# Kernel tuning notes

Measured on AMD Instinct MI355X. Metric: run time of the kernel, lower is better.

The kernel has to match this reference:

```python
import jax, jax.numpy as jnp
import numpy as np

B, T, D, H = 4096, 512, 8, 64  # batch, seq_len, input_size, hidden_size


def setup_inputs() -> dict:
    key = jax.random.key(0)
    ks = jax.random.split(key, 11)
    s = lambda k, shape: (jax.random.normal(k, shape, dtype=jnp.float32) * 0.1)
    return {
        "x": jax.random.normal(ks[0], (B, T, D), dtype=jnp.float32),
        # layer 0 (input_size -> H), PyTorch gate order i,f,g,o packed along 4H
        "Wih0": s(ks[1], (4 * H, D)),
        "Whh0": s(ks[2], (4 * H, H)),
        "bih0": s(ks[3], (4 * H,)),
        "bhh0": s(ks[4], (4 * H,)),
        # layer 1 (H -> H)
        "Wih1": s(ks[5], (4 * H, H)),
        "Whh1": s(ks[6], (4 * H, H)),
        "bih1": s(ks[7], (4 * H,)),
        "bhh1": s(ks[8], (4 * H,)),
        # final linear head H -> 1
        "Wfc": s(ks[9], (1, H)),
        "bfc": s(ks[10], (1,)),
    }


def _lstm_layer(x, Wih, Whh, bih, bhh):
    """Single-direction LSTM layer over x:[B,T,Din] -> hs:[B,T,H]."""
    b, t, _ = x.shape
    h_dim = Whh.shape[1]
    # Precompute input contribution for all timesteps (one big GEMM).
    xg = jnp.einsum("btd,gd->btg", x, Wih) + bih + bhh  # [B,T,4H]

    def step(carry, gx_t):
        h, c = carry
        z = gx_t + h @ Whh.T  # [B,4H]
        i, f, g, o = jnp.split(z, 4, axis=-1)
        i = jax.nn.sigmoid(i)
        f = jax.nn.sigmoid(f)
        g = jnp.tanh(g)
        o = jax.nn.sigmoid(o)
        c = f * c + i * g
        h = o * jnp.tanh(c)
        return (h, c), h

    h0 = jnp.zeros((b, h_dim), x.dtype)
    c0 = jnp.zeros((b, h_dim), x.dtype)
    (_, _), hs = jax.lax.scan(step, (h0, c0), jnp.swapaxes(xg, 0, 1))
    return jnp.swapaxes(hs, 0, 1)  # [B,T,H]


def reference(x, Wih0, Whh0, bih0, bhh0, Wih1, Whh1, bih1, bhh1, Wfc, bfc):
    # nn.LSTM with num_layers=2, batch_first=True; dropout inactive in eval.
    h1 = _lstm_layer(x, Wih0, Whh0, bih0, bhh0)
    h2 = _lstm_layer(h1, Wih1, Whh1, bih1, bhh1)
    last = h2[:, -1, :]  # [B,H]
    return last @ Wfc.T + bfc  # [B,1]
```

## Files before the change

### kernel.cpp

```cpp
#include <hip/hip_runtime.h>

#define BTOT 4096
#define TB   512
#define BD   8
#define BSL  16

#define A0TOG  1024
#define A1BASE 2048
#define A1TOG  1024
#define ZBASE  4096
#define XBASE  8192
#define NLDS   24576

typedef __attribute__((ext_vector_type(8))) short  short8;
typedef __attribute__((ext_vector_type(4))) float  f32x4;

static __device__ __forceinline__ unsigned short f2bf(float f) {
    unsigned u = __float_as_uint(f);
    u += 0x7fffu + ((u >> 16) & 1u);
    return (unsigned short)(u >> 16);
}
static __device__ __forceinline__ float bf2f(unsigned short h) {
    return __uint_as_float(((unsigned)h) << 16);
}
static __device__ __forceinline__ unsigned pkbf(float a, float b) {
    unsigned r;
    asm("v_cvt_pk_bf16_f32 %0, %1, %2" : "=v"(r) : "v"(a), "v"(b));
    return r;
}

static __device__ __forceinline__ void gates4(
    const f32x4 ai, const f32x4 af, const f32x4 ag, const f32x4 ao,
    float cc[4], unsigned hp[2])
{
    float h[4];
    #pragma unroll
    for (int r = 0; r < 4; ++r) {
        const float ei = __builtin_amdgcn_exp2f(ai[r]);
        const float ef = __builtin_amdgcn_exp2f(af[r]);
        const float eg = __builtin_amdgcn_exp2f(ag[r]);
        const float eo = __builtin_amdgcn_exp2f(ao[r]);
        const float Ai = 1.f + ei, Af = 1.f + ef, Ag = 1.f + eg, Ao = 1.f + eo;
        const float P    = Ai * Ag;
        const float numer = cc[r] * P + Af * (eg - 1.f);
        const float rD   = __builtin_amdgcn_rcpf(Af * P);
        cc[r] = numer * rD;
        const float ec = __builtin_amdgcn_exp2f(2.88539008f * cc[r]);
        const float rH = __builtin_amdgcn_rcpf(Ao * (ec + 1.f));
        h[r] = (ec - 1.f) * rH;
    }
    hp[0] = pkbf(h[0], h[1]); hp[1] = pkbf(h[2], h[3]);
}

__global__ __launch_bounds__(512, 2) void lstm2_fused(
    const float* __restrict__ x,
    const float* __restrict__ Wih0, const float* __restrict__ Whh0,
    const float* __restrict__ bih0, const float* __restrict__ bhh0,
    const float* __restrict__ Wih1, const float* __restrict__ Whh1,
    const float* __restrict__ bih1, const float* __restrict__ bhh1,
    const float* __restrict__ Wfc,  const float* __restrict__ bfc,
    float* __restrict__ out)
{
    __shared__ __align__(16) unsigned short lds16[NLDS];

    const int tid  = threadIdx.x;
    const int wid  = tid >> 6;
    const int lane = tid & 63;
    const int q    = lane >> 4;
    const int ln   = lane & 15;
    const int rb   = blockIdx.x * BSL;

    const bool L1w = (wid >= 4);
    const int  g   = L1w ? (wid - 4) : wid;
    const int  jc  = g * 16 + ln;

    const float SCI = -1.44269504f;
    const float SCG =  2.88539008f;
    short8 Bf[4][4];
    #pragma unroll
    for (int G = 0; G < 4; ++G) {
        const int n = G * 64 + jc;
        const float sc = (G == 2) ? SCG : SCI;
        #pragma unroll
        for (int ki = 0; ki < 4; ++ki) {
            union { unsigned short u[8]; short8 v; } t;
            #pragma unroll
            for (int j = 0; j < 8; ++j) {
                const int k = ki * 32 + q * 8 + j;
                float wv = 0.0f;
                if (!L1w) {
                    if (ki < 3) {
                        if (k < 64)      wv = Whh0[n * 64 + k];
                        else if (k < 72) wv = Wih0[n * 8 + (k - 64)];
                    }
                } else {
                    if (k < 64)          wv = Wih1[n * 64 + k];
                    else                 wv = Whh1[n * 64 + (k - 64)];
                }
                t.u[j] = f2bf(sc * wv);
            }
            Bf[G][ki] = t.v;
        }
    }
    f32x4 biasv[4];
    #pragma unroll
    for (int G = 0; G < 4; ++G) {
        const int n = G * 64 + jc;
        const float sc = (G == 2) ? SCG : SCI;
        const float b = sc * (L1w ? (bih1[n] + bhh1[n]) : (bih0[n] + bhh0[n]));
        biasv[G] = (f32x4){b, b, b, b};
    }

    {
        unsigned* z = (unsigned*)lds16;
        #pragma unroll
        for (int i = 0; i < 5; ++i) {
            const int id = tid + i * 512;
            if (id < 2112) z[id] = 0;
        }
    }
    const int srow = tid >> 5, su = tid & 31;
    {
        const float* gp = x + (size_t)(rb + srow) * (TB * BD) + su * 16;
        const float4 v0 = ((const float4*)gp)[0];
        const float4 v1 = ((const float4*)gp)[1];
        const float4 v2 = ((const float4*)gp)[2];
        const float4 v3 = ((const float4*)gp)[3];
        uint4 s0, s1;
        s0.x = pkbf(v0.x, v0.y); s0.y = pkbf(v0.z, v0.w);
        s0.z = pkbf(v1.x, v1.y); s0.w = pkbf(v1.z, v1.w);
        s1.x = pkbf(v2.x, v2.y); s1.y = pkbf(v2.z, v2.w);
        s1.z = pkbf(v3.x, v3.y); s1.w = pkbf(v3.z, v3.w);
        const int el = XBASE + (su * 2) * 128 + srow * 8;
        *(uint4*)(lds16 + el)       = s0;
        *(uint4*)(lds16 + el + 128) = s1;
    }
    __syncthreads();

    const int rbase = q * 128 + ln * 8;
    const int wb    = (jc >> 3) * 128 + q * 32 + (jc & 7);
    const int ln8   = ln * 8;
    const int zaddr = ZBASE + ln8;
    int rdA  = rbase;
    int wr0  = A0TOG + wb;
    int rdH0 = rbase;
    int rdH1 = A1BASE + rbase;
    int wrH1 = A1BASE + A1TOG + wb;

    float cc[4] = {0.f, 0.f, 0.f, 0.f};
    float4 px0, px1, px2, px3;

    for (int it = 0; it <= TB; ++it) {
        const int ph = it & 63;
        if (ph == 48 && it + 16 < TB) {
            const int t0 = (it & ~63) + 64;
            const float* gp = x + (size_t)(rb + srow) * (TB * BD) + t0 * BD + su * 16;
            px0 = ((const float4*)gp)[0];
            px1 = ((const float4*)gp)[1];
            px2 = ((const float4*)gp)[2];
            px3 = ((const float4*)gp)[3];
        }
        if (ph == 62 && it + 2 < TB) {
            const int t0 = (it & ~63) + 64;
            uint4 s0, s1;
            s0.x = pkbf(px0.x, px0.y); s0.y = pkbf(px0.z, px0.w);
            s0.z = pkbf(px1.x, px1.y); s0.w = pkbf(px1.z, px1.w);
            s1.x = pkbf(px2.x, px2.y); s1.y = pkbf(px2.z, px2.w);
            s1.z = pkbf(px3.x, px3.y); s1.w = pkbf(px3.z, px3.w);
            const int el = XBASE + ((t0 & 127) + su * 2) * 128 + srow * 8;
            *(uint4*)(lds16 + el)       = s0;
            *(uint4*)(lds16 + el + 128) = s1;
        }

        if (!L1w) {
            if (it < TB) {
                const short8 a0 = *(const short8*)(lds16 + rdA);
                const short8 a1 = *(const short8*)(lds16 + rdA + 512);
                const int xaddr = (q == 0) ? (XBASE + ((it & 127) << 7) + ln8) : zaddr;
                const short8 a2 = *(const short8*)(lds16 + xaddr);

                f32x4 ai = __builtin_amdgcn_mfma_f32_16x16x32_bf16(a0, Bf[0][0], biasv[0], 0, 0, 0);
                f32x4 af = __builtin_amdgcn_mfma_f32_16x16x32_bf16(a0, Bf[1][0], biasv[1], 0, 0, 0);
                f32x4 ag = __builtin_amdgcn_mfma_f32_16x16x32_bf16(a0, Bf[2][0], biasv[2], 0, 0, 0);
                f32x4 ao = __builtin_amdgcn_mfma_f32_16x16x32_bf16(a0, Bf[3][0], biasv[3], 0, 0, 0);
                ai = __builtin_amdgcn_mfma_f32_16x16x32_bf16(a1, Bf[0][1], ai, 0, 0, 0);
                af = __builtin_amdgcn_mfma_f32_16x16x32_bf16(a1, Bf[1][1], af, 0, 0, 0);
                ag = __builtin_amdgcn_mfma_f32_16x16x32_bf16(a1, Bf[2][1], ag, 0, 0, 0);
                ao = __builtin_amdgcn_mfma_f32_16x16x32_bf16(a1, Bf[3][1], ao, 0, 0, 0);
                ai = __builtin_amdgcn_mfma_f32_16x16x32_bf16(a2, Bf[0][2], ai, 0, 0, 0);
                af = __builtin_amdgcn_mfma_f32_16x16x32_bf16(a2, Bf[1][2], af, 0, 0, 0);
                ag = __builtin_amdgcn_mfma_f32_16x16x32_bf16(a2, Bf[2][2], ag, 0, 0, 0);
                ao = __builtin_amdgcn_mfma_f32_16x16x32_bf16(a2, Bf[3][2], ao, 0, 0, 0);

                unsigned hp[2];
                gates4(ai, af, ag, ao, cc, hp);
                lds16[wr0]      = (unsigned short)hp[0];
                lds16[wr0 + 8]  = (unsigned short)(hp[0] >> 16);
                lds16[wr0 + 16] = (unsigned short)hp[1];
                lds16[wr0 + 24] = (unsigned short)(hp[1] >> 16);
            }
        } else {
            if (it >= 1) {
                const short8 a0 = *(const short8*)(lds16 + rdH0);
                const short8 a1 = *(const short8*)(lds16 + rdH0 + 512);
                const short8 a2 = *(const short8*)(lds16 + rdH1);
                const short8 a3 = *(const short8*)(lds16 + rdH1 + 512);

                f32x4 ai = __builtin_amdgcn_mfma_f32_16x16x32_bf16(a0, Bf[0][0], biasv[0], 0, 0, 0);
                f32x4 af = __builtin_amdgcn_mfma_f32_16x16x32_bf16(a0, Bf[1][0], biasv[1], 0, 0, 0);
                f32x4 ag = __builtin_amdgcn_mfma_f32_16x16x32_bf16(a0, Bf[2][0], biasv[2], 0, 0, 0);
                f32x4 ao = __builtin_amdgcn_mfma_f32_16x16x32_bf16(a0, Bf[3][0], biasv[3], 0, 0, 0);
                ai = __builtin_amdgcn_mfma_f32_16x16x32_bf16(a1, Bf[0][1], ai, 0, 0, 0);
                af = __builtin_amdgcn_mfma_f32_16x16x32_bf16(a1, Bf[1][1], af, 0, 0, 0);
                ag = __builtin_amdgcn_mfma_f32_16x16x32_bf16(a1, Bf[2][1], ag, 0, 0, 0);
                ao = __builtin_amdgcn_mfma_f32_16x16x32_bf16(a1, Bf[3][1], ao, 0, 0, 0);
                ai = __builtin_amdgcn_mfma_f32_16x16x32_bf16(a2, Bf[0][2], ai, 0, 0, 0);
                af = __builtin_amdgcn_mfma_f32_16x16x32_bf16(a2, Bf[1][2], af, 0, 0, 0);
                ag = __builtin_amdgcn_mfma_f32_16x16x32_bf16(a2, Bf[2][2], ag, 0, 0, 0);
                ao = __builtin_amdgcn_mfma_f32_16x16x32_bf16(a2, Bf[3][2], ao, 0, 0, 0);
                ai = __builtin_amdgcn_mfma_f32_16x16x32_bf16(a3, Bf[0][3], ai, 0, 0, 0);
                af = __builtin_amdgcn_mfma_f32_16x16x32_bf16(a3, Bf[1][3], af, 0, 0, 0);
                ag = __builtin_amdgcn_mfma_f32_16x16x32_bf16(a3, Bf[2][3], ag, 0, 0, 0);
                ao = __builtin_amdgcn_mfma_f32_16x16x32_bf16(a3, Bf[3][3], ao, 0, 0, 0);

                unsigned hp[2];
                gates4(ai, af, ag, ao, cc, hp);
                lds16[wrH1]      = (unsigned short)hp[0];
                lds16[wrH1 + 8]  = (unsigned short)(hp[0] >> 16);
                lds16[wrH1 + 16] = (unsigned short)hp[1];
                lds16[wrH1 + 24] = (unsigned short)(hp[1] >> 16);
            }
        }
        __syncthreads();
        rdA ^= A0TOG; wr0 ^= A0TOG; rdH0 ^= A0TOG;
        rdH1 ^= A1TOG; wrH1 ^= A1TOG;
    }

    if (tid < BSL) {
        float s = bfc[0];
        #pragma unroll 8
        for (int j = 0; j < 64; ++j)
            s += bf2f(lds16[A1BASE + A1TOG + (j >> 3) * 128 + tid * 8 + (j & 7)]) * Wfc[j];
        out[rb + tid] = s;
    }
}

extern "C" void kernel_launch(void* const* d_in, const int* in_sizes, int n_in,
                              void* d_out, int out_size, void* d_ws, size_t ws_size,
                              hipStream_t stream) {
    const float* x    = (const float*)d_in[0];
    const float* Wih0 = (const float*)d_in[1];
    const float* Whh0 = (const float*)d_in[2];
    const float* bih0 = (const float*)d_in[3];
    const float* bhh0 = (const float*)d_in[4];
    const float* Wih1 = (const float*)d_in[5];
    const float* Whh1 = (const float*)d_in[6];
    const float* bih1 = (const float*)d_in[7];
    const float* bhh1 = (const float*)d_in[8];
    const float* Wfc  = (const float*)d_in[9];
    const float* bfc  = (const float*)d_in[10];
    float* out = (float*)d_out;

    dim3 grid(BTOT / BSL);
    dim3 block(512);
    lstm2_fused<<<grid, block, 0, stream>>>(x, Wih0, Whh0, bih0, bhh0,
                                            Wih1, Whh1, bih1, bhh1, Wfc, bfc, out);
}
```

Measured before the change: 503.6 us.

## Replace per-step block barriers with LDS progress flags and 4-deep h ring buffers

Replaces the per-timestep __syncthreads with per-wave progress counters in LDS that each wave spins on, so layer-0 and layer-1 waves can run decoupled by up to a few steps. Hidden states move to four-slot ring buffers per layer so producers can run ahead without overwriting data still being read. The x prefetch is also remapped so only 256 threads load 4 timesteps each. This trades barrier stalls for spin-polling LDS traffic and extra LDS use, and relies on fences and volatile reads for correctness.

```diff
diff --git a/kernel.cpp b/kernel.cpp
--- a/kernel.cpp
+++ b/kernel.cpp
@@ -5,12 +5,11 @@
 #define BD   8
 #define BSL  16
 
-#define A0TOG  1024
-#define A1BASE 2048
-#define A1TOG  1024
-#define ZBASE  4096
-#define XBASE  8192
-#define NLDS   24576
+#define H1R    4096
+#define ZBASE  8192
+#define PROGEL 8320
+#define XBASE  12288
+#define NLDS   28672
 
 typedef __attribute__((ext_vector_type(8))) short  short8;
 typedef __attribute__((ext_vector_type(4))) float  f32x4;
@@ -27,6 +26,11 @@
     unsigned r;
     asm("v_cvt_pk_bf16_f32 %0, %1, %2" : "=v"(r) : "v"(a), "v"(b));
     return r;
+}
+static __device__ __forceinline__ unsigned min4h(unsigned a, unsigned b) {
+    const unsigned m1 = min(a & 0xffffu, a >> 16);
+    const unsigned m2 = min(b & 0xffffu, b >> 16);
+    return min(m1, m2);
 }
 
 static __device__ __forceinline__ void gates4(
@@ -41,9 +45,9 @@
         const float eg = __builtin_amdgcn_exp2f(ag[r]);
         const float eo = __builtin_amdgcn_exp2f(ao[r]);
         const float Ai = 1.f + ei, Af = 1.f + ef, Ag = 1.f + eg, Ao = 1.f + eo;
-        const float P    = Ai * Ag;
+        const float P = Ai * Ag;
         const float numer = cc[r] * P + Af * (eg - 1.f);
-        const float rD   = __builtin_amdgcn_rcpf(Af * P);
+        const float rD = __builtin_amdgcn_rcpf(Af * P);
         cc[r] = numer * rD;
         const float ec = __builtin_amdgcn_exp2f(2.88539008f * cc[r]);
         const float rH = __builtin_amdgcn_rcpf(Ao * (ec + 1.f));
@@ -113,134 +117,148 @@
 
     {
         unsigned* z = (unsigned*)lds16;
+        z[1536 + tid] = 0;
+        z[3584 + tid] = 0;
+        if (tid < 64) z[4096 + tid] = 0;
+        if (tid < 4)
+            z[4160 + tid] = (tid >= 2) ? 0x00010001u : 0u;
+    }
+    const int srow = (tid >> 4) & 15, su = tid & 15;
+    if (tid < 256) {
+        const float* gp = x + (size_t)(rb + srow) * (TB * BD) + (su * 4) * BD;
+        float4 v[8];
         #pragma unroll
-        for (int i = 0; i < 5; ++i) {
-            const int id = tid + i * 512;
-            if (id < 2112) z[id] = 0;
-        }
-    }
-    const int srow = tid >> 5, su = tid & 31;
-    {
-        const float* gp = x + (size_t)(rb + srow) * (TB * BD) + su * 16;
-        const float4 v0 = ((const float4*)gp)[0];
-        const float4 v1 = ((const float4*)gp)[1];
-        const float4 v2 = ((const float4*)gp)[2];
-        const float4 v3 = ((const float4*)gp)[3];
-        uint4 s0, s1;
-        s0.x = pkbf(v0.x, v0.y); s0.y = pkbf(v0.z, v0.w);
-        s0.z = pkbf(v1.x, v1.y); s0.w = pkbf(v1.z, v1.w);
-        s1.x = pkbf(v2.x, v2.y); s1.y = pkbf(v2.z, v2.w);
-        s1.z = pkbf(v3.x, v3.y); s1.w = pkbf(v3.z, v3.w);
-        const int el = XBASE + (su * 2) * 128 + srow * 8;
-        *(uint4*)(lds16 + el)       = s0;
-        *(uint4*)(lds16 + el + 128) = s1;
+        for (int i = 0; i < 8; ++i) v[i] = ((const float4*)gp)[i];
+        #pragma unroll
+        for (int tt = 0; tt < 4; ++tt) {
+            uint4 s;
+            s.x = pkbf(v[tt*2].x, v[tt*2].y);   s.y = pkbf(v[tt*2].z, v[tt*2].w);
+            s.z = pkbf(v[tt*2+1].x, v[tt*2+1].y); s.w = pkbf(v[tt*2+1].z, v[tt*2+1].w);
+            *(uint4*)(lds16 + XBASE + (su * 4 + tt) * 128 + srow * 8) = s;
+        }
     }
     __syncthreads();
 
     const int rbase = q * 128 + ln * 8;
     const int wb    = (jc >> 3) * 128 + q * 32 + (jc & 7);
     const int ln8   = ln * 8;
-    const int zaddr = ZBASE + ln8;
-    int rdA  = rbase;
-    int wr0  = A0TOG + wb;
-    int rdH0 = rbase;
-    int rdH1 = A1BASE + rbase;
-    int wrH1 = A1BASE + A1TOG + wb;
+    volatile unsigned* pr = (volatile unsigned*)(lds16 + PROGEL);
 
     float cc[4] = {0.f, 0.f, 0.f, 0.f};
-    float4 px0, px1, px2, px3;
-
-    for (int it = 0; it <= TB; ++it) {
-        const int ph = it & 63;
-        if (ph == 48 && it + 16 < TB) {
-            const int t0 = (it & ~63) + 64;
-            const float* gp = x + (size_t)(rb + srow) * (TB * BD) + t0 * BD + su * 16;
-            px0 = ((const float4*)gp)[0];
-            px1 = ((const float4*)gp)[1];
-            px2 = ((const float4*)gp)[2];
-            px3 = ((const float4*)gp)[3];
-        }
-        if (ph == 62 && it + 2 < TB) {
-            const int t0 = (it & ~63) + 64;
-            uint4 s0, s1;
-            s0.x = pkbf(px0.x, px0.y); s0.y = pkbf(px0.z, px0.w);
-            s0.z = pkbf(px1.x, px1.y); s0.w = pkbf(px1.z, px1.w);
-            s1.x = pkbf(px2.x, px2.y); s1.y = pkbf(px2.z, px2.w);
-            s1.z = pkbf(px3.x, px3.y); s1.w = pkbf(px3.z, px3.w);
-            const int el = XBASE + ((t0 & 127) + su * 2) * 128 + srow * 8;
-            *(uint4*)(lds16 + el)       = s0;
-            *(uint4*)(lds16 + el + 128) = s1;
-        }
-
-        if (!L1w) {
-            if (it < TB) {
-                const short8 a0 = *(const short8*)(lds16 + rdA);
-                const short8 a1 = *(const short8*)(lds16 + rdA + 512);
-                const int xaddr = (q == 0) ? (XBASE + ((it & 127) << 7) + ln8) : zaddr;
-                const short8 a2 = *(const short8*)(lds16 + xaddr);
-
-                f32x4 ai = __builtin_amdgcn_mfma_f32_16x16x32_bf16(a0, Bf[0][0], biasv[0], 0, 0, 0);
-                f32x4 af = __builtin_amdgcn_mfma_f32_16x16x32_bf16(a0, Bf[1][0], biasv[1], 0, 0, 0);
-                f32x4 ag = __builtin_amdgcn_mfma_f32_16x16x32_bf16(a0, Bf[2][0], biasv[2], 0, 0, 0);
-                f32x4 ao = __builtin_amdgcn_mfma_f32_16x16x32_bf16(a0, Bf[3][0], biasv[3], 0, 0, 0);
-                ai = __builtin_amdgcn_mfma_f32_16x16x32_bf16(a1, Bf[0][1], ai, 0, 0, 0);
-                af = __builtin_amdgcn_mfma_f32_16x16x32_bf16(a1, Bf[1][1], af, 0, 0, 0);
-                ag = __builtin_amdgcn_mfma_f32_16x16x32_bf16(a1, Bf[2][1], ag, 0, 0, 0);
-                ao = __builtin_amdgcn_mfma_f32_16x16x32_bf16(a1, Bf[3][1], ao, 0, 0, 0);
-                ai = __builtin_amdgcn_mfma_f32_16x16x32_bf16(a2, Bf[0][2], ai, 0, 0, 0);
-                af = __builtin_amdgcn_mfma_f32_16x16x32_bf16(a2, Bf[1][2], af, 0, 0, 0);
-                ag = __builtin_amdgcn_mfma_f32_16x16x32_bf16(a2, Bf[2][2], ag, 0, 0, 0);
-                ao = __builtin_amdgcn_mfma_f32_16x16x32_bf16(a2, Bf[3][2], ao, 0, 0, 0);
-
-                unsigned hp[2];
-                gates4(ai, af, ag, ao, cc, hp);
-                lds16[wr0]      = (unsigned short)hp[0];
-                lds16[wr0 + 8]  = (unsigned short)(hp[0] >> 16);
-                lds16[wr0 + 16] = (unsigned short)hp[1];
-                lds16[wr0 + 24] = (unsigned short)(hp[1] >> 16);
-            }
-        } else {
-            if (it >= 1) {
-                const short8 a0 = *(const short8*)(lds16 + rdH0);
-                const short8 a1 = *(const short8*)(lds16 + rdH0 + 512);
-                const short8 a2 = *(const short8*)(lds16 + rdH1);
-                const short8 a3 = *(const short8*)(lds16 + rdH1 + 512);
-
-                f32x4 ai = __builtin_amdgcn_mfma_f32_16x16x32_bf16(a0, Bf[0][0], biasv[0], 0, 0, 0);
-                f32x4 af = __builtin_amdgcn_mfma_f32_16x16x32_bf16(a0, Bf[1][0], biasv[1], 0, 0, 0);
-                f32x4 ag = __builtin_amdgcn_mfma_f32_16x16x32_bf16(a0, Bf[2][0], biasv[2], 0, 0, 0);
-                f32x4 ao = __builtin_amdgcn_mfma_f32_16x16x32_bf16(a0, Bf[3][0], biasv[3], 0, 0, 0);
-                ai = __builtin_amdgcn_mfma_f32_16x16x32_bf16(a1, Bf[0][1], ai, 0, 0, 0);
-                af = __builtin_amdgcn_mfma_f32_16x16x32_bf16(a1, Bf[1][1], af, 0, 0, 0);
-                ag = __builtin_amdgcn_mfma_f32_16x16x32_bf16(a1, Bf[2][1], ag, 0, 0, 0);
-                ao = __builtin_amdgcn_mfma_f32_16x16x32_bf16(a1, Bf[3][1], ao, 0, 0, 0);
-                ai = __builtin_amdgcn_mfma_f32_16x16x32_bf16(a2, Bf[0][2], ai, 0, 0, 0);
-                af = __builtin_amdgcn_mfma_f32_16x16x32_bf16(a2, Bf[1][2], af, 0, 0, 0);
-                ag = __builtin_amdgcn_mfma_f32_16x16x32_bf16(a2, Bf[2][2], ag, 0, 0, 0);
-                ao = __builtin_amdgcn_mfma_f32_16x16x32_bf16(a2, Bf[3][2], ao, 0, 0, 0);
-                ai = __builtin_amdgcn_mfma_f32_16x16x32_bf16(a3, Bf[0][3], ai, 0, 0, 0);
-                af = __builtin_amdgcn_mfma_f32_16x16x32_bf16(a3, Bf[1][3], af, 0, 0, 0);
-                ag = __builtin_amdgcn_mfma_f32_16x16x32_bf16(a3, Bf[2][3], ag, 0, 0, 0);
-                ao = __builtin_amdgcn_mfma_f32_16x16x32_bf16(a3, Bf[3][3], ao, 0, 0, 0);
-
-                unsigned hp[2];
-                gates4(ai, af, ag, ao, cc, hp);
-                lds16[wrH1]      = (unsigned short)hp[0];
-                lds16[wrH1 + 8]  = (unsigned short)(hp[0] >> 16);
-                lds16[wrH1 + 16] = (unsigned short)hp[1];
-                lds16[wrH1 + 24] = (unsigned short)(hp[1] >> 16);
-            }
-        }
-        __syncthreads();
-        rdA ^= A0TOG; wr0 ^= A0TOG; rdH0 ^= A0TOG;
-        rdH1 ^= A1TOG; wrH1 ^= A1TOG;
-    }
+
+    if (!L1w) {
+        float4 px[8];
+        for (int it = 0; it < TB; ++it) {
+            const int ph = it & 63;
+            if (ph == 48 && it + 16 < TB) {
+                const int t0 = (it & ~63) + 64;
+                const float* gp = x + (size_t)(rb + srow) * (TB * BD) + (t0 + su * 4) * BD;
+                #pragma unroll
+                for (int i = 0; i < 8; ++i) px[i] = ((const float4*)gp)[i];
+            }
+            if (ph == 62 && it + 2 < TB) {
+                const int t0 = (it & ~63) + 64;
+                #pragma unroll
+                for (int tt = 0; tt < 4; ++tt) {
+                    uint4 s;
+                    s.x = pkbf(px[tt*2].x, px[tt*2].y);     s.y = pkbf(px[tt*2].z, px[tt*2].w);
+                    s.z = pkbf(px[tt*2+1].x, px[tt*2+1].y); s.w = pkbf(px[tt*2+1].z, px[tt*2+1].w);
+                    *(uint4*)(lds16 + XBASE + ((t0 & 127) + su * 4 + tt) * 128 + srow * 8) = s;
+                }
+            }
+            {
+                const unsigned tg0 = (unsigned)it;
+                const unsigned tg1 = (it >= 2) ? (unsigned)(it - 2) : 0u;
+                while (true) {
+                    const unsigned p0 = pr[0], p1 = pr[1], p2 = pr[2], p3 = pr[3];
+                    if (min4h(p0, p1) >= tg0 && min4h(p2, p3) >= tg1) break;
+                }
+                asm volatile("" ::: "memory");
+            }
+            const int rs = ((it + 3) & 3) << 10;
+            const short8 a0 = *(const short8*)(lds16 + rs + rbase);
+            const short8 a1 = *(const short8*)(lds16 + rs + rbase + 512);
+            const int xaddr = (q == 0) ? (XBASE + ((it & 127) << 7) + ln8) : (ZBASE + ln8);
+            const short8 a2 = *(const short8*)(lds16 + xaddr);
+
+            f32x4 ai = __builtin_amdgcn_mfma_f32_16x16x32_bf16(a0, Bf[0][0], biasv[0], 0, 0, 0);
+            f32x4 af = __builtin_amdgcn_mfma_f32_16x16x32_bf16(a0, Bf[1][0], biasv[1], 0, 0, 0);
+            f32x4 ag = __builtin_amdgcn_mfma_f32_16x16x32_bf16(a0, Bf[2][0], biasv[2], 0, 0, 0);
+            f32x4 ao = __builtin_amdgcn_mfma_f32_16x16x32_bf16(a0, Bf[3][0], biasv[3], 0, 0, 0);
+            ai = __builtin_amdgcn_mfma_f32_16x16x32_bf16(a1, Bf[0][1], ai, 0, 0, 0);
+            af = __builtin_amdgcn_mfma_f32_16x16x32_bf16(a1, Bf[1][1], af, 0, 0, 0);
+            ag = __builtin_amdgcn_mfma_f32_16x16x32_bf16(a1, Bf[2][1], ag, 0, 0, 0);
+            ao = __builtin_amdgcn_mfma_f32_16x16x32_bf16(a1, Bf[3][1], ao, 0, 0, 0);
+            ai = __builtin_amdgcn_mfma_f32_16x16x32_bf16(a2, Bf[0][2], ai, 0, 0, 0);
+            af = __builtin_amdgcn_mfma_f32_16x16x32_bf16(a2, Bf[1][2], af, 0, 0, 0);
+            ag = __builtin_amdgcn_mfma_f32_16x16x32_bf16(a2, Bf[2][2], ag, 0, 0, 0);
+            ao = __builtin_amdgcn_mfma_f32_16x16x32_bf16(a2, Bf[3][2], ao, 0, 0, 0);
+
+            unsigned hp[2];
+            gates4(ai, af, ag, ao, cc, hp);
+            const int ws = (it & 3) << 10;
+            lds16[ws + wb]      = (unsigned short)hp[0];
+            lds16[ws + wb + 8]  = (unsigned short)(hp[0] >> 16);
+            lds16[ws + wb + 16] = (unsigned short)hp[1];
+            lds16[ws + wb + 24] = (unsigned short)(hp[1] >> 16);
+            __threadfence_block();
+            if (lane == 0)
+                *(volatile unsigned short*)(lds16 + PROGEL + wid) = (unsigned short)(it + 1);
+        }
+    } else {
+        for (int it = 1; it <= TB; ++it) {
+            {
+                const unsigned tg = (unsigned)it;
+                while (true) {
+                    const unsigned p0 = pr[0], p1 = pr[1], p2 = pr[2], p3 = pr[3];
+                    if (min4h(p0, p1) >= tg && min4h(p2, p3) >= tg) break;
+                }
+                asm volatile("" ::: "memory");
+            }
+            const int rs0 = ((it + 3) & 3) << 10;
+            const int rs1 = H1R + (((it + 2) & 3) << 10);
+            const short8 a0 = *(const short8*)(lds16 + rs0 + rbase);
+            const short8 a1 = *(const short8*)(lds16 + rs0 + rbase + 512);
+            const short8 a2 = *(const short8*)(lds16 + rs1 + rbase);
+            const short8 a3 = *(const short8*)(lds16 + rs1 + rbase + 512);
+
+            f32x4 ai = __builtin_amdgcn_mfma_f32_16x16x32_bf16(a0, Bf[0][0], biasv[0], 0, 0, 0);
+            f32x4 af = __builtin_amdgcn_mfma_f32_16x16x32_bf16(a0, Bf[1][0], biasv[1], 0, 0, 0);
+            f32x4 ag = __builtin_amdgcn_mfma_f32_16x16x32_bf16(a0, Bf[2][0], biasv[2], 0, 0, 0);
+            f32x4 ao = __builtin_amdgcn_mfma_f32_16x16x32_bf16(a0, Bf[3][0], biasv[3], 0, 0, 0);
+            ai = __builtin_amdgcn_mfma_f32_16x16x32_bf16(a1, Bf[0][1], ai, 0, 0, 0);
+            af = __builtin_amdgcn_mfma_f32_16x16x32_bf16(a1, Bf[1][1], af, 0, 0, 0);
+            ag = __builtin_amdgcn_mfma_f32_16x16x32_bf16(a1, Bf[2][1], ag, 0, 0, 0);
+            ao = __builtin_amdgcn_mfma_f32_16x16x32_bf16(a1, Bf[3][1], ao, 0, 0, 0);
+            ai = __builtin_amdgcn_mfma_f32_16x16x32_bf16(a2, Bf[0][2], ai, 0, 0, 0);
+            af = __builtin_amdgcn_mfma_f32_16x16x32_bf16(a2, Bf[1][2], af, 0, 0, 0);
+            ag = __builtin_amdgcn_mfma_f32_16x16x32_bf16(a2, Bf[2][2], ag, 0, 0, 0);
+            ao = __builtin_amdgcn_mfma_f32_16x16x32_bf16(a2, Bf[3][2], ao, 0, 0, 0);
+            ai = __builtin_amdgcn_mfma_f32_16x16x32_bf16(a3, Bf[0][3], ai, 0, 0, 0);
+            af = __builtin_amdgcn_mfma_f32_16x16x32_bf16(a3, Bf[1][3], af, 0, 0, 0);
+            ag = __builtin_amdgcn_mfma_f32_16x16x32_bf16(a3, Bf[2][3], ag, 0, 0, 0);
+            ao = __builtin_amdgcn_mfma_f32_16x16x32_bf16(a3, Bf[3][3], ao, 0, 0, 0);
+
+            unsigned hp[2];
+            gates4(ai, af, ag, ao, cc, hp);
+            const int ws = H1R + (((it + 3) & 3) << 10);
+            lds16[ws + wb]      = (unsigned short)hp[0];
+            lds16[ws + wb + 8]  = (unsigned short)(hp[0] >> 16);
+            lds16[ws + wb + 16] = (unsigned short)hp[1];
+            lds16[ws + wb + 24] = (unsigned short)(hp[1] >> 16);
+            __threadfence_block();
+            if (lane == 0)
+                *(volatile unsigned short*)(lds16 + PROGEL + wid) = (unsigned short)(it + 1);
+        }
+    }
+
+    __syncthreads();
 
     if (tid < BSL) {
         float s = bfc[0];
         #pragma unroll 8
         for (int j = 0; j < 64; ++j)
-            s += bf2f(lds16[A1BASE + A1TOG + (j >> 3) * 128 + tid * 8 + (j & 7)]) * Wfc[j];
+            s += bf2f(lds16[H1R + 3072 + (j >> 3) * 128 + tid * 8 + (j & 7)]) * Wfc[j];
         out[rb + tid] = s;
     }
 }
```

Result: slower. 561.3 us (+11.5%).
